# Kernel optimization log

Measured on AMD Instinct MI355X. Metric: run time of the kernel, lower is better.

Reference implementation:

```python
import jax, jax.numpy as jnp
import numpy as np

E = 4096      # hidden_size
H = 32        # num_attention_heads
D = E // H    # head_dim = 128
PAST = 8191   # past kv length


def setup_inputs() -> dict:
    key = jax.random.key(0)
    ks = jax.random.split(key, 10)
    s = 0.02
    return {
        "hidden_states": jax.random.normal(ks[0], (1, 1, E), jnp.float32),
        "past_key": jax.random.normal(ks[1], (1, D, PAST), jnp.float32),
        "past_value": jax.random.normal(ks[2], (1, PAST, D), jnp.float32),
        "attention_mask": jnp.zeros((1, 1, 1, PAST + 1), jnp.float32),
        "q_w": jax.random.normal(ks[3], (E, E), jnp.float32) * s,
        "q_b": jnp.zeros((E,), jnp.float32),
        "kv_w": jax.random.normal(ks[4], (E, 2 * D), jnp.float32) * s,
        "kv_b": jnp.zeros((2 * D,), jnp.float32),
        "proj_w": jax.random.normal(ks[5], (E, E), jnp.float32) * s,
        "proj_b": jnp.zeros((E,), jnp.float32),
    }


def reference(hidden_states, past_key, past_value, attention_mask,
              q_w, q_b, kv_w, kv_b, proj_w, proj_b):
    B, S = hidden_states.shape[:2]  # B=1, S=1 (decode)
    # Conv1D projections: x @ W + b
    query = hidden_states @ q_w + q_b            # [B, S, E]
    kv = hidden_states @ kv_w + kv_b             # [B, S, 2D]
    key_new, value_new = kv[..., :D], kv[..., D:]  # [B, S, D] each

    q = query.reshape(B, S, H, D).transpose(0, 2, 1, 3)  # [B, H, S, D]
    key_perm = key_new.transpose(0, 2, 1)                 # [B, D, S]
    full_key = jnp.concatenate([past_key, key_perm], axis=-1)     # [B, D, K]
    full_value = jnp.concatenate([past_value, value_new], axis=-2)  # [B, K, D]
    K = full_key.shape[-1]

    # QK^T with shared single KV head, scaled by sqrt(head_dim)
    scores = jnp.einsum('bhqd,bdk->bhqk', q, full_key)  # [B, H, S, K]
    scores = scores / jnp.asarray(D ** 0.5, scores.dtype)

    # causal mask over rows [K-S, K)
    causal = (jnp.arange(K)[None, :] <= (jnp.arange(S) + (K - S))[:, None])  # [S, K]
    mask_value = jnp.asarray(jnp.finfo(scores.dtype).min, scores.dtype)
    scores = jnp.where(causal[None, None], scores, mask_value)
    scores = scores + attention_mask

    attn_weights = jax.nn.softmax(scores, axis=-1)                # [B, H, S, K]
    attn_out = jnp.einsum('bhqk,bkd->bhqd', attn_weights, full_value)  # [B, H, S, D]
    attn_out = attn_out.transpose(0, 2, 1, 3).reshape(B, S, E)    # merge heads
    attn_out = attn_out @ proj_w + proj_b                          # [B, S, E]
    return attn_out, key_perm, value_new
```

## Files before the change

kernel.cpp:

```cpp
#include <hip/hip_runtime.h>
#include <math.h>

#define E_DIM 4096
#define H_NUM 32
#define D_DIM 128
#define PAST_K 8191
#define K_TOT 8192

#define WS_QUERY 0
#define WS_KV    4096
#define WS_PQ    4608
#define WS_PA    (WS_PQ + 256*4352)
#define WS_PL    (WS_PA + 128*4096)
#define WS_PP    (WS_PL + 4096)

__global__ void k_qkv(const float* __restrict__ hs,
                      const float* __restrict__ q_w,
                      const float* __restrict__ kv_w,
                      float* __restrict__ ws) {
    const int t = threadIdx.x;
    const int e0 = blockIdx.y * 16;
    if (blockIdx.x < 4) {
        const int o = blockIdx.x * 1024 + t * 4;
        float ax = 0.f, ay = 0.f, az = 0.f, aw = 0.f;
#pragma unroll
        for (int i = 0; i < 16; ++i) {
            const int e = e0 + i;
            const float x = hs[e];
            const float4 w = *reinterpret_cast<const float4*>(q_w + (size_t)e * E_DIM + o);
            ax += x * w.x; ay += x * w.y; az += x * w.z; aw += x * w.w;
        }
        *reinterpret_cast<float4*>(ws + WS_PQ + (size_t)blockIdx.y * 4352 + o) =
            make_float4(ax, ay, az, aw);
    } else {
        if (t >= 64) return;
        const int o = t * 4;
        float ax = 0.f, ay = 0.f, az = 0.f, aw = 0.f;
#pragma unroll
        for (int i = 0; i < 16; ++i) {
            const int e = e0 + i;
            const float x = hs[e];
            const float4 w = *reinterpret_cast<const float4*>(kv_w + (size_t)e * 256 + o);
            ax += x * w.x; ay += x * w.y; az += x * w.z; aw += x * w.w;
        }
        *reinterpret_cast<float4*>(ws + WS_PQ + (size_t)blockIdx.y * 4352 + 4096 + o) =
            make_float4(ax, ay, az, aw);
    }
}

__global__ void k_qkv_reduce(const float* __restrict__ q_b, const float* __restrict__ kv_b,
                             float* __restrict__ ws, float* __restrict__ out) {
    __shared__ float rr[256];
    const int t = threadIdx.x;
    const int ol = t & 63;
    const int sg = t >> 6;
    const int o = blockIdx.x * 64 + ol;
    float acc = 0.f;
#pragma unroll 8
    for (int s = sg * 64; s < sg * 64 + 64; ++s)
        acc += ws[WS_PQ + (size_t)s * 4352 + o];
    rr[sg * 64 + ol] = acc;
    __syncthreads();
    if (t < 64) {
        float v = rr[ol] + rr[64 + ol] + rr[128 + ol] + rr[192 + ol];
        const int oo = blockIdx.x * 64 + ol;
        if (oo < 4096) {
            ws[WS_QUERY + oo] = v + q_b[oo];
        } else {
            const int i = oo - 4096;
            const float r = v + kv_b[i];
            ws[WS_KV + i] = r;
            out[oo] = r;
        }
    }
}

__global__ void __launch_bounds__(512, 4)
k_attn(const float* __restrict__ past_key,
       const float* __restrict__ past_value,
       const float* __restrict__ mask,
       float* __restrict__ ws) {
    __shared__ float sq[4 * 128];
    __shared__ float sp[4 * 64];
    __shared__ float red[2048];
    const int t = threadIdx.x;
    const int hy = blockIdx.y;
    const int kx = blockIdx.x;
    const int h0 = hy * 4;
    const int k0 = kx * 64;
    const float* __restrict__ kvn = ws + WS_KV;

    sq[t] = ws[WS_QUERY + h0 * D_DIM + t];
    __syncthreads();

    const int kl = t & 63;
    const int team = t >> 6;
    const int d0 = team * 16;
    const int k = k0 + kl;
    const bool tailA = (k == PAST_K);
    const float* kp = tailA ? (kvn + d0) : (past_key + (size_t)d0 * PAST_K + k);
    const size_t kstr = tailA ? 1 : PAST_K;

    float a0 = 0.f, a1 = 0.f, a2 = 0.f, a3 = 0.f;
#pragma unroll
    for (int i = 0; i < 16; i += 4) {
        const float v0 = kp[0];
        const float v1 = kp[kstr];
        const float v2 = kp[2 * kstr];
        const float v3 = kp[3 * kstr];
        kp += 4 * kstr;
        const float4 q0 = *reinterpret_cast<const float4*>(&sq[0 * 128 + d0 + i]);
        const float4 q1 = *reinterpret_cast<const float4*>(&sq[1 * 128 + d0 + i]);
        const float4 q2 = *reinterpret_cast<const float4*>(&sq[2 * 128 + d0 + i]);
        const float4 q3 = *reinterpret_cast<const float4*>(&sq[3 * 128 + d0 + i]);
        a0 += q0.x * v0 + q0.y * v1 + q0.z * v2 + q0.w * v3;
        a1 += q1.x * v0 + q1.y * v1 + q1.z * v2 + q1.w * v3;
        a2 += q2.x * v0 + q2.y * v1 + q2.z * v2 + q2.w * v3;
        a3 += q3.x * v0 + q3.y * v1 + q3.z * v2 + q3.w * v3;
    }
    if (team != 0) {
        red[((team - 1) * 4 + 0) * 64 + kl] = a0;
        red[((team - 1) * 4 + 1) * 64 + kl] = a1;
        red[((team - 1) * 4 + 2) * 64 + kl] = a2;
        red[((team - 1) * 4 + 3) * 64 + kl] = a3;
    }
    __syncthreads();
    if (team == 0) {
        const float scale = 0.08838834764831845f;
        const float mk = mask[k];
        float s0 = a0, s1 = a1, s2 = a2, s3 = a3;
#pragma unroll
        for (int tm = 0; tm < 7; ++tm) {
            s0 += red[(tm * 4 + 0) * 64 + kl];
            s1 += red[(tm * 4 + 1) * 64 + kl];
            s2 += red[(tm * 4 + 2) * 64 + kl];
            s3 += red[(tm * 4 + 3) * 64 + kl];
        }
        const float e0 = __expf(s0 * scale + mk);
        const float e1 = __expf(s1 * scale + mk);
        const float e2 = __expf(s2 * scale + mk);
        const float e3 = __expf(s3 * scale + mk);
        sp[0 * 64 + kl] = e0;
        sp[1 * 64 + kl] = e1;
        sp[2 * 64 + kl] = e2;
        sp[3 * 64 + kl] = e3;
        float l0 = e0, l1 = e1, l2 = e2, l3 = e3;
#pragma unroll
        for (int off = 32; off > 0; off >>= 1) {
            l0 += __shfl_xor(l0, off);
            l1 += __shfl_xor(l1, off);
            l2 += __shfl_xor(l2, off);
            l3 += __shfl_xor(l3, off);
        }
        if (t == 0) {
            float* pl = ws + WS_PL + ((size_t)(kx * 8 + hy)) * 4;
            pl[0] = l0; pl[1] = l1; pl[2] = l2; pl[3] = l3;
        }
    }
    __syncthreads();

    const int d = t & 127;
    const int kg = t >> 7;
    const int kb = k0 + kg * 16;
    const float* __restrict__ vp = past_value + (size_t)kb * D_DIM + d;
    const float* __restrict__ vlast =
        (kb + 15 == PAST_K) ? (kvn + D_DIM + d) : (vp + 15 * (size_t)D_DIM);

    float b0 = 0.f, b1 = 0.f, b2 = 0.f, b3 = 0.f;
#pragma unroll
    for (int kk = 0; kk < 15; ++kk) {
        const float v = vp[(size_t)kk * D_DIM];
        b0 += sp[0 * 64 + kg * 16 + kk] * v;
        b1 += sp[1 * 64 + kg * 16 + kk] * v;
        b2 += sp[2 * 64 + kg * 16 + kk] * v;
        b3 += sp[3 * 64 + kg * 16 + kk] * v;
    }
    {
        const float v = *vlast;
        b0 += sp[0 * 64 + kg * 16 + 15] * v;
        b1 += sp[1 * 64 + kg * 16 + 15] * v;
        b2 += sp[2 * 64 + kg * 16 + 15] * v;
        b3 += sp[3 * 64 + kg * 16 + 15] * v;
    }
    __syncthreads();
    red[(kg * 4 + 0) * 128 + d] = b0;
    red[(kg * 4 + 1) * 128 + d] = b1;
    red[(kg * 4 + 2) * 128 + d] = b2;
    red[(kg * 4 + 3) * 128 + d] = b3;
    __syncthreads();

    const int hh = t >> 7;
    const float s = red[(0 * 4 + hh) * 128 + d] + red[(1 * 4 + hh) * 128 + d] +
                    red[(2 * 4 + hh) * 128 + d] + red[(3 * 4 + hh) * 128 + d];
    ws[WS_PA + (size_t)kx * 4096 + (h0 + hh) * D_DIM + d] = s;
}

__global__ void k_proj(const float* __restrict__ proj_w,
                       float* __restrict__ ws) {
    __shared__ float sred[16 * 16];
    __shared__ float lpart[2];
    __shared__ float sa[16];
    const int t = threadIdx.x;
    const int by = blockIdx.y;
    const int e0 = by * 16;
    const int h  = by >> 3;
    const int hy = h >> 2;
    const int hh = h & 3;

    {
        const int el = t & 15;
        const int kg = t >> 4;
        float ps = 0.f;
#pragma unroll
        for (int j = 0; j < 8; ++j)
            ps += ws[WS_PA + (size_t)(kg * 8 + j) * 4096 + e0 + el];
        sred[kg * 16 + el] = ps;
    }
    if (t < 128) {
        float lv = ws[WS_PL + ((size_t)(t * 8 + hy)) * 4 + hh];
#pragma unroll
        for (int off = 32; off > 0; off >>= 1) lv += __shfl_xor(lv, off);
        if ((t & 63) == 0) lpart[t >> 6] = lv;
    }
    __syncthreads();
    if (t < 16) {
        float asum = 0.f;
#pragma unroll
        for (int g = 0; g < 16; ++g) asum += sred[g * 16 + t];
        sa[t] = asum / (lpart[0] + lpart[1]);
    }
    __syncthreads();

    const int o = blockIdx.x * 1024 + t * 4;
    float ax = 0.f, ay = 0.f, az = 0.f, aw = 0.f;
#pragma unroll
    for (int i = 0; i < 16; ++i) {
        const float x = sa[i];
        const float4 w = *reinterpret_cast<const float4*>(proj_w + (size_t)(e0 + i) * E_DIM + o);
        ax += x * w.x; ay += x * w.y; az += x * w.z; aw += x * w.w;
    }
    *reinterpret_cast<float4*>(ws + WS_PP + (size_t)by * 4096 + o) =
        make_float4(ax, ay, az, aw);
}

__global__ void k_proj_reduce(const float* __restrict__ proj_b,
                              float* __restrict__ ws, float* __restrict__ out) {
    __shared__ float rr[256];
    const int t = threadIdx.x;
    const int ol = t & 63;
    const int sg = t >> 6;
    const int o = blockIdx.x * 64 + ol;
    float acc = 0.f;
#pragma unroll 8
    for (int s = sg * 64; s < sg * 64 + 64; ++s)
        acc += ws[WS_PP + (size_t)s * 4096 + o];
    rr[sg * 64 + ol] = acc;
    __syncthreads();
    if (t < 64) {
        const int oo = blockIdx.x * 64 + ol;
        out[oo] = rr[ol] + rr[64 + ol] + rr[128 + ol] + rr[192 + ol] + proj_b[oo];
    }
}

extern "C" void kernel_launch(void* const* d_in, const int* in_sizes, int n_in,
                              void* d_out, int out_size, void* d_ws, size_t ws_size,
                              hipStream_t stream) {
    const float* hs      = (const float*)d_in[0];
    const float* past_k  = (const float*)d_in[1];
    const float* past_v  = (const float*)d_in[2];
    const float* mask    = (const float*)d_in[3];
    const float* q_w     = (const float*)d_in[4];
    const float* q_b     = (const float*)d_in[5];
    const float* kv_w    = (const float*)d_in[6];
    const float* kv_b    = (const float*)d_in[7];
    const float* proj_w  = (const float*)d_in[8];
    const float* proj_b  = (const float*)d_in[9];
    float* out = (float*)d_out;
    float* ws  = (float*)d_ws;

    k_qkv        <<<dim3(5, 256), dim3(256), 0, stream>>>(hs, q_w, kv_w, ws);
    k_qkv_reduce <<<dim3(68),     dim3(256), 0, stream>>>(q_b, kv_b, ws, out);
    k_attn       <<<dim3(128, 8), dim3(512), 0, stream>>>(past_k, past_v, mask, ws);
    k_proj       <<<dim3(4, 256), dim3(256), 0, stream>>>(proj_w, ws);
    k_proj_reduce<<<dim3(64),     dim3(256), 0, stream>>>(proj_b, ws, out);
}
```

Measured before the change: 201.1 us.

## Process eight heads per attention block and widen GEMV blocks

Each attention block now handles eight query heads instead of four, so every past key/value element loaded from memory feeds twice as many dot products and the KV cache is read half as many times overall. The QKV and projection GEMV kernels move to 512-thread blocks covering 2048 outputs, and both reduction kernels use 32 outputs per block, giving twice as many blocks. In exchange the attention kernel carries more accumulators and shared memory, which lowers occupancy, and it launches half as many blocks.

```diff
diff --git a/kernel.cpp b/kernel.cpp
--- a/kernel.cpp
+++ b/kernel.cpp
@@ -14,14 +14,15 @@
 #define WS_PL    (WS_PA + 128*4096)
 #define WS_PP    (WS_PL + 4096)
 
-__global__ void k_qkv(const float* __restrict__ hs,
-                      const float* __restrict__ q_w,
-                      const float* __restrict__ kv_w,
-                      float* __restrict__ ws) {
+__global__ void __launch_bounds__(512, 2)
+k_qkv(const float* __restrict__ hs,
+      const float* __restrict__ q_w,
+      const float* __restrict__ kv_w,
+      float* __restrict__ ws) {
     const int t = threadIdx.x;
     const int e0 = blockIdx.y * 16;
-    if (blockIdx.x < 4) {
-        const int o = blockIdx.x * 1024 + t * 4;
+    if (blockIdx.x < 2) {
+        const int o = blockIdx.x * 2048 + t * 4;
         float ax = 0.f, ay = 0.f, az = 0.f, aw = 0.f;
 #pragma unroll
         for (int i = 0; i < 16; ++i) {
@@ -48,22 +49,25 @@
     }
 }
 
-__global__ void k_qkv_reduce(const float* __restrict__ q_b, const float* __restrict__ kv_b,
-                             float* __restrict__ ws, float* __restrict__ out) {
+__global__ void __launch_bounds__(256, 4)
+k_qkv_reduce(const float* __restrict__ q_b, const float* __restrict__ kv_b,
+             float* __restrict__ ws, float* __restrict__ out) {
     __shared__ float rr[256];
     const int t = threadIdx.x;
-    const int ol = t & 63;
-    const int sg = t >> 6;
-    const int o = blockIdx.x * 64 + ol;
+    const int ol = t & 31;
+    const int sg = t >> 5;
+    const int o = blockIdx.x * 32 + ol;
     float acc = 0.f;
 #pragma unroll 8
-    for (int s = sg * 64; s < sg * 64 + 64; ++s)
+    for (int s = sg * 32; s < sg * 32 + 32; ++s)
         acc += ws[WS_PQ + (size_t)s * 4352 + o];
-    rr[sg * 64 + ol] = acc;
-    __syncthreads();
-    if (t < 64) {
-        float v = rr[ol] + rr[64 + ol] + rr[128 + ol] + rr[192 + ol];
-        const int oo = blockIdx.x * 64 + ol;
+    rr[t] = acc;
+    __syncthreads();
+    if (t < 32) {
+        float v = 0.f;
+#pragma unroll
+        for (int g = 0; g < 8; ++g) v += rr[g * 32 + t];
+        const int oo = blockIdx.x * 32 + t;
         if (oo < 4096) {
             ws[WS_QUERY + oo] = v + q_b[oo];
         } else {
@@ -75,22 +79,23 @@
     }
 }
 
-__global__ void __launch_bounds__(512, 4)
+__global__ void __launch_bounds__(512, 2)
 k_attn(const float* __restrict__ past_key,
        const float* __restrict__ past_value,
        const float* __restrict__ mask,
        float* __restrict__ ws) {
-    __shared__ float sq[4 * 128];
-    __shared__ float sp[4 * 64];
-    __shared__ float red[2048];
+    __shared__ float sq[8 * 128];
+    __shared__ float sp[8 * 64];
+    __shared__ float red[3584];
     const int t = threadIdx.x;
     const int hy = blockIdx.y;
     const int kx = blockIdx.x;
-    const int h0 = hy * 4;
+    const int h0 = hy * 8;
     const int k0 = kx * 64;
     const float* __restrict__ kvn = ws + WS_KV;
 
-    sq[t] = ws[WS_QUERY + h0 * D_DIM + t];
+    sq[t]       = ws[WS_QUERY + h0 * D_DIM + t];
+    sq[t + 512] = ws[WS_QUERY + h0 * D_DIM + t + 512];
     __syncthreads();
 
     const int kl = t & 63;
@@ -101,7 +106,10 @@
     const float* kp = tailA ? (kvn + d0) : (past_key + (size_t)d0 * PAST_K + k);
     const size_t kstr = tailA ? 1 : PAST_K;
 
-    float a0 = 0.f, a1 = 0.f, a2 = 0.f, a3 = 0.f;
+    float acc[8];
+#pragma unroll
+    for (int h = 0; h < 8; ++h) acc[h] = 0.f;
+
 #pragma unroll
     for (int i = 0; i < 16; i += 4) {
         const float v0 = kp[0];
@@ -109,52 +117,40 @@
         const float v2 = kp[2 * kstr];
         const float v3 = kp[3 * kstr];
         kp += 4 * kstr;
-        const float4 q0 = *reinterpret_cast<const float4*>(&sq[0 * 128 + d0 + i]);
-        const float4 q1 = *reinterpret_cast<const float4*>(&sq[1 * 128 + d0 + i]);
-        const float4 q2 = *reinterpret_cast<const float4*>(&sq[2 * 128 + d0 + i]);
-        const float4 q3 = *reinterpret_cast<const float4*>(&sq[3 * 128 + d0 + i]);
-        a0 += q0.x * v0 + q0.y * v1 + q0.z * v2 + q0.w * v3;
-        a1 += q1.x * v0 + q1.y * v1 + q1.z * v2 + q1.w * v3;
-        a2 += q2.x * v0 + q2.y * v1 + q2.z * v2 + q2.w * v3;
-        a3 += q3.x * v0 + q3.y * v1 + q3.z * v2 + q3.w * v3;
+#pragma unroll
+        for (int h = 0; h < 8; ++h) {
+            const float4 q = *reinterpret_cast<const float4*>(&sq[h * 128 + d0 + i]);
+            acc[h] += q.x * v0 + q.y * v1 + q.z * v2 + q.w * v3;
+        }
     }
     if (team != 0) {
-        red[((team - 1) * 4 + 0) * 64 + kl] = a0;
-        red[((team - 1) * 4 + 1) * 64 + kl] = a1;
-        red[((team - 1) * 4 + 2) * 64 + kl] = a2;
-        red[((team - 1) * 4 + 3) * 64 + kl] = a3;
+#pragma unroll
+        for (int h = 0; h < 8; ++h)
+            red[((team - 1) * 8 + h) * 64 + kl] = acc[h];
     }
     __syncthreads();
     if (team == 0) {
         const float scale = 0.08838834764831845f;
         const float mk = mask[k];
-        float s0 = a0, s1 = a1, s2 = a2, s3 = a3;
-#pragma unroll
-        for (int tm = 0; tm < 7; ++tm) {
-            s0 += red[(tm * 4 + 0) * 64 + kl];
-            s1 += red[(tm * 4 + 1) * 64 + kl];
-            s2 += red[(tm * 4 + 2) * 64 + kl];
-            s3 += red[(tm * 4 + 3) * 64 + kl];
-        }
-        const float e0 = __expf(s0 * scale + mk);
-        const float e1 = __expf(s1 * scale + mk);
-        const float e2 = __expf(s2 * scale + mk);
-        const float e3 = __expf(s3 * scale + mk);
-        sp[0 * 64 + kl] = e0;
-        sp[1 * 64 + kl] = e1;
-        sp[2 * 64 + kl] = e2;
-        sp[3 * 64 + kl] = e3;
-        float l0 = e0, l1 = e1, l2 = e2, l3 = e3;
-#pragma unroll
-        for (int off = 32; off > 0; off >>= 1) {
-            l0 += __shfl_xor(l0, off);
-            l1 += __shfl_xor(l1, off);
-            l2 += __shfl_xor(l2, off);
-            l3 += __shfl_xor(l3, off);
+        float l[8];
+#pragma unroll
+        for (int h = 0; h < 8; ++h) {
+            float s = acc[h];
+#pragma unroll
+            for (int tm = 0; tm < 7; ++tm) s += red[(tm * 8 + h) * 64 + kl];
+            const float e = __expf(s * scale + mk);
+            sp[h * 64 + kl] = e;
+            l[h] = e;
+        }
+#pragma unroll
+        for (int h = 0; h < 8; ++h) {
+#pragma unroll
+            for (int off = 32; off > 0; off >>= 1) l[h] += __shfl_xor(l[h], off);
         }
         if (t == 0) {
-            float* pl = ws + WS_PL + ((size_t)(kx * 8 + hy)) * 4;
-            pl[0] = l0; pl[1] = l1; pl[2] = l2; pl[3] = l3;
+            float* pl = ws + WS_PL + ((size_t)(kx * 4 + hy)) * 8;
+#pragma unroll
+            for (int h = 0; h < 8; ++h) pl[h] = l[h];
         }
     }
     __syncthreads();
@@ -166,58 +162,60 @@
     const float* __restrict__ vlast =
         (kb + 15 == PAST_K) ? (kvn + D_DIM + d) : (vp + 15 * (size_t)D_DIM);
 
-    float b0 = 0.f, b1 = 0.f, b2 = 0.f, b3 = 0.f;
+    float b[8];
+#pragma unroll
+    for (int h = 0; h < 8; ++h) b[h] = 0.f;
+
 #pragma unroll
     for (int kk = 0; kk < 15; ++kk) {
         const float v = vp[(size_t)kk * D_DIM];
-        b0 += sp[0 * 64 + kg * 16 + kk] * v;
-        b1 += sp[1 * 64 + kg * 16 + kk] * v;
-        b2 += sp[2 * 64 + kg * 16 + kk] * v;
-        b3 += sp[3 * 64 + kg * 16 + kk] * v;
+#pragma unroll
+        for (int h = 0; h < 8; ++h) b[h] += sp[h * 64 + kg * 16 + kk] * v;
     }
     {
         const float v = *vlast;
-        b0 += sp[0 * 64 + kg * 16 + 15] * v;
-        b1 += sp[1 * 64 + kg * 16 + 15] * v;
-        b2 += sp[2 * 64 + kg * 16 + 15] * v;
-        b3 += sp[3 * 64 + kg * 16 + 15] * v;
-    }
-    __syncthreads();
-    red[(kg * 4 + 0) * 128 + d] = b0;
-    red[(kg * 4 + 1) * 128 + d] = b1;
-    red[(kg * 4 + 2) * 128 + d] = b2;
-    red[(kg * 4 + 3) * 128 + d] = b3;
-    __syncthreads();
-
-    const int hh = t >> 7;
-    const float s = red[(0 * 4 + hh) * 128 + d] + red[(1 * 4 + hh) * 128 + d] +
-                    red[(2 * 4 + hh) * 128 + d] + red[(3 * 4 + hh) * 128 + d];
-    ws[WS_PA + (size_t)kx * 4096 + (h0 + hh) * D_DIM + d] = s;
-}
-
-__global__ void k_proj(const float* __restrict__ proj_w,
-                       float* __restrict__ ws) {
-    __shared__ float sred[16 * 16];
+#pragma unroll
+        for (int h = 0; h < 8; ++h) b[h] += sp[h * 64 + kg * 16 + 15] * v;
+    }
+    __syncthreads();
+    if (kg != 0) {
+#pragma unroll
+        for (int h = 0; h < 8; ++h)
+            red[((kg - 1) * 8 + h) * 128 + d] = b[h];
+    }
+    __syncthreads();
+    if (kg == 0) {
+#pragma unroll
+        for (int h = 0; h < 8; ++h) {
+            float s = b[h] + red[(0 * 8 + h) * 128 + d] +
+                      red[(1 * 8 + h) * 128 + d] + red[(2 * 8 + h) * 128 + d];
+            ws[WS_PA + (size_t)kx * 4096 + (h0 + h) * D_DIM + d] = s;
+        }
+    }
+}
+
+__global__ void __launch_bounds__(512, 2)
+k_proj(const float* __restrict__ proj_w,
+       float* __restrict__ ws) {
+    __shared__ float sred[32 * 16];
     __shared__ float lpart[2];
     __shared__ float sa[16];
     const int t = threadIdx.x;
     const int by = blockIdx.y;
     const int e0 = by * 16;
     const int h  = by >> 3;
-    const int hy = h >> 2;
-    const int hh = h & 3;
 
     {
         const int el = t & 15;
         const int kg = t >> 4;
         float ps = 0.f;
 #pragma unroll
-        for (int j = 0; j < 8; ++j)
-            ps += ws[WS_PA + (size_t)(kg * 8 + j) * 4096 + e0 + el];
+        for (int j = 0; j < 4; ++j)
+            ps += ws[WS_PA + (size_t)(kg * 4 + j) * 4096 + e0 + el];
         sred[kg * 16 + el] = ps;
     }
     if (t < 128) {
-        float lv = ws[WS_PL + ((size_t)(t * 8 + hy)) * 4 + hh];
+        float lv = ws[WS_PL + (size_t)t * 32 + (h >> 3) * 8 + (h & 7)];
 #pragma unroll
         for (int off = 32; off > 0; off >>= 1) lv += __shfl_xor(lv, off);
         if ((t & 63) == 0) lpart[t >> 6] = lv;
@@ -226,12 +224,12 @@
     if (t < 16) {
         float asum = 0.f;
 #pragma unroll
-        for (int g = 0; g < 16; ++g) asum += sred[g * 16 + t];
+        for (int g = 0; g < 32; ++g) asum += sred[g * 16 + t];
         sa[t] = asum / (lpart[0] + lpart[1]);
     }
     __syncthreads();
 
-    const int o = blockIdx.x * 1024 + t * 4;
+    const int o = blockIdx.x * 2048 + t * 4;
     float ax = 0.f, ay = 0.f, az = 0.f, aw = 0.f;
 #pragma unroll
     for (int i = 0; i < 16; ++i) {
@@ -243,22 +241,26 @@
         make_float4(ax, ay, az, aw);
 }
 
-__global__ void k_proj_reduce(const float* __restrict__ proj_b,
-                              float* __restrict__ ws, float* __restrict__ out) {
+__global__ void __launch_bounds__(256, 4)
+k_proj_reduce(const float* __restrict__ proj_b,
+              float* __restrict__ ws, float* __restrict__ out) {
     __shared__ float rr[256];
     const int t = threadIdx.x;
-    const int ol = t & 63;
-    const int sg = t >> 6;
-    const int o = blockIdx.x * 64 + ol;
+    const int ol = t & 31;
+    const int sg = t >> 5;
+    const int o = blockIdx.x * 32 + ol;
     float acc = 0.f;
 #pragma unroll 8
-    for (int s = sg * 64; s < sg * 64 + 64; ++s)
+    for (int s = sg * 32; s < sg * 32 + 32; ++s)
         acc += ws[WS_PP + (size_t)s * 4096 + o];
-    rr[sg * 64 + ol] = acc;
-    __syncthreads();
-    if (t < 64) {
-        const int oo = blockIdx.x * 64 + ol;
-        out[oo] = rr[ol] + rr[64 + ol] + rr[128 + ol] + rr[192 + ol] + proj_b[oo];
+    rr[t] = acc;
+    __syncthreads();
+    if (t < 32) {
+        float v = 0.f;
+#pragma unroll
+        for (int g = 0; g < 8; ++g) v += rr[g * 32 + t];
+        const int oo = blockIdx.x * 32 + t;
+        out[oo] = v + proj_b[oo];
     }
 }
 
@@ -278,9 +280,9 @@
     float* out = (float*)d_out;
     float* ws  = (float*)d_ws;
 
-    k_qkv        <<<dim3(5, 256), dim3(256), 0, stream>>>(hs, q_w, kv_w, ws);
-    k_qkv_reduce <<<dim3(68),     dim3(256), 0, stream>>>(q_b, kv_b, ws, out);
-    k_attn       <<<dim3(128, 8), dim3(512), 0, stream>>>(past_k, past_v, mask, ws);
-    k_proj       <<<dim3(4, 256), dim3(256), 0, stream>>>(proj_w, ws);
-    k_proj_reduce<<<dim3(64),     dim3(256), 0, stream>>>(proj_b, ws, out);
-}
+    k_qkv        <<<dim3(3, 256), dim3(512), 0, stream>>>(hs, q_w, kv_w, ws);
+    k_qkv_reduce <<<dim3(136),    dim3(256), 0, stream>>>(q_b, kv_b, ws, out);
+    k_attn       <<<dim3(128, 4), dim3(512), 0, stream>>>(past_k, past_v, mask, ws);
+    k_proj       <<<dim3(2, 256), dim3(512), 0, stream>>>(proj_w, ws);
+    k_proj_reduce<<<dim3(128),    dim3(256), 0, stream>>>(proj_b, ws, out);
+}
```

Result: faster. 194.9 us (-3.1%).
